# Performance work log

Hardware: AMD Instinct MI355X
Metric: run time of the kernel (lower is better)

Reference implementation:

```python
import jax, jax.numpy as jnp
import numpy as np
from jax import lax

# Module config (matches init_kwargs): mode='swta', patchwise=True, w_nrm=True, k=1, alpha=1
COUT, CIN, KH, KW = 32, 16, 3, 3
STRIDE = 1
K_TEMP = 1.0


def setup_inputs() -> dict:
    key = jax.random.key(0)
    k1, k2 = jax.random.split(key)
    x = jax.random.normal(k1, (16, CIN, 256, 256), dtype=jnp.float32)
    # xavier_normal_: std = sqrt(2/(fan_in+fan_out)), fan_in=CIN*KH*KW, fan_out=COUT*KH*KW
    std = float(np.sqrt(2.0 / (CIN * KH * KW + COUT * KH * KW)))
    weight = jax.random.normal(k2, (COUT, CIN, KH, KW), dtype=jnp.float32) * std
    bias = jnp.zeros((COUT,), dtype=jnp.float32)
    return {"x": x, "weight": weight, "bias": bias}


def _unfold(x, kh, kw, sh, sw):
    # torch F.unfold: output [B, C*kh*kw, L], patch features ordered (c, kh, kw)
    B, C, H, W = x.shape
    Ho = (H - kh) // sh + 1
    Wo = (W - kw) // sw + 1
    cols = [x[:, :, i:i + (Ho - 1) * sh + 1:sh, j:j + (Wo - 1) * sw + 1:sw]
            for i in range(kh) for j in range(kw)]  # each [B,C,Ho,Wo]
    p = jnp.stack(cols, axis=2)  # [B, C, kh*kw, Ho, Wo]
    return p.reshape(B, C * kh * kw, Ho * Wo)


def reference(x, weight, bias):
    # --- compute_activation: weight-normalized conv2d (act = Identity) ---
    nrm = jnp.sqrt((weight ** 2).sum(axis=(1, 2, 3), keepdims=True))
    nrm = jnp.where(nrm == 0, jnp.ones_like(nrm), nrm)
    w = weight / nrm
    y = lax.conv_general_dilated(
        x, w, window_strides=(STRIDE, STRIDE), padding='VALID',
        dimension_numbers=('NCHW', 'OIHW', 'NCHW')) + bias[None, :, None, None]

    # --- SWTA Hebbian update (torch: under no_grad, stored into delta_w buffer) ---
    x_unf = _unfold(x, KH, KW, STRIDE, STRIDE)               # [B, CKK, L]
    x_flat = x_unf.transpose(0, 2, 1).reshape(-1, x_unf.shape[1])  # [B*L, CKK]
    r = jax.nn.softmax(y * K_TEMP, axis=1).transpose(1, 0, 2, 3)   # [O, B, Ho, Wo]
    r_sum = jnp.abs(r).sum(axis=(1, 2, 3), keepdims=True)
    r_sum = jnp.where(r_sum == 0, jnp.ones_like(r_sum), r_sum)
    cr = (jnp.abs(r) / r_sum) * r                             # [O, B, Ho, Wo]
    cr_flat = cr.reshape(COUT, -1)                            # [O, B*L]
    dec = cr_flat.sum(axis=1, keepdims=True) * weight.reshape(COUT, -1)
    delta_w = (cr_flat @ x_flat - dec).reshape(weight.shape)  # [O, CIN, KH, KW]

    return y, delta_w
```

## Files before the change

### kernel.cpp

```cpp
#include <hip/hip_runtime.h>


typedef unsigned short ushort_t;
typedef __attribute__((ext_vector_type(8)))  short  short8v;
typedef __attribute__((ext_vector_type(4)))  float  float4v;
typedef __attribute__((ext_vector_type(16))) float  float16v;

struct __attribute__((packed, aligned(4))) f4a { float x,y,z,w; };
struct __attribute__((packed, aligned(4))) f2a { float x,y; };
struct __attribute__((packed, aligned(2))) u2a { ushort_t x,y; };

#define BATCH 16
#define CIN   16
#define H     256
#define W     256
#define HW    (H*W)
#define OCH   32
#define HO    254
#define WO    254
#define LPOS  (HO*WO)
#define YELEMS (BATCH*OCH*LPOS)
#define KFEAT 144
#define NROWS (BATCH*HO)
#define NCHUNK (NROWS*8)
#define GRIDA 1016
#define NSLAB GRIDA
#define NGRP  8
#define SLABS_PER_GRP 127

#define WS_RSUM 0
#define WS_R2   32
#define WS_ACC  64
#define WS_MODE 4672
#define WS_WNB  4680
#define WS_PART 8192
#define WS_PART2 (8192 + NSLAB*4608)
#define WS_NEED ((size_t)(WS_PART2 + NGRP*4608)*4)

__device__ __forceinline__ float bf2f(ushort_t u){
  union{unsigned u; float f;} c; c.u = ((unsigned)u) << 16; return c.f;
}
__device__ __forceinline__ ushort_t f2bf(float f){
  union{float f; unsigned u;} c; c.f = f;
  unsigned x = c.u;
  return (ushort_t)((x + 0x7fffu + ((x >> 16) & 1u)) >> 16);
}
__device__ __forceinline__ unsigned as_u(float f){
  union{float f; unsigned u;} c; c.f = f; return c.u;
}

__global__ __launch_bounds__(256) void hebb_prep(const ushort_t* __restrict__ x,
                                                 const ushort_t* __restrict__ w,
                                                 int* __restrict__ mode,
                                                 float* __restrict__ ws){
  int tid = threadIdx.x;
  int bad = 0;
  for (int i = tid; i < 16384; i += 256){
    unsigned e = ((unsigned)x[i] >> 7) & 0xFFu;
    bad |= (e >= 0x8Cu) ? 1 : 0;
  }
  unsigned long long m = __ballot(bad);
  __shared__ unsigned long long sm[4];
  __shared__ int mode_s;
  int wv = tid >> 6;
  if ((tid & 63) == 0) sm[wv] = m;
  __syncthreads();
  if (tid == 0){
    int md = ((sm[0] | sm[1] | sm[2] | sm[3]) != 0ULL) ? 1 : 0;
    *mode = md; mode_s = md;
  }
  __syncthreads();
  const int fp32 = mode_s;
  const float* wf = (const float*)w;
  __shared__ float inv_s[OCH];
  if (tid < OCH){
    float s = 0.f;
    for (int k = 0; k < KFEAT; k++){
      float v = fp32 ? wf[tid*KFEAT + k] : bf2f(w[tid*KFEAT + k]);
      s += v*v;
    }
    float nrm = sqrtf(s);
    inv_s[tid] = (nrm == 0.f) ? 1.f : (1.f/nrm);
  }
  __syncthreads();
  ushort_t* wnb = (ushort_t*)(ws + WS_WNB);
  for (int i = tid; i < 4608; i += 256){
    int o = i & 31, rest = i >> 5;
    int ij = rest >> 4, c = rest & 15;
    int k = c*9 + ij;
    float v = fp32 ? wf[o*KFEAT + k] : bf2f(w[o*KFEAT + k]);
    wnb[i] = f2bf(v * inv_s[o]);
    ws[WS_ACC + i] = 0.f;
  }
  if (tid < 64) ws[WS_RSUM + tid] = 0.f;
}

template<int FP32>
__global__ __launch_bounds__(256, 2) void hebb_passAB(
    const void* __restrict__ xv_, const void* __restrict__ bias_,
    const int* __restrict__ mode, const float* __restrict__ ws,
    float* __restrict__ rsum_g, float* __restrict__ r2sum_g,
    void* __restrict__ yout_, float* __restrict__ partial, int do_hebb){
  if (*mode != FP32) return;
  __shared__ float red_s[64];
  __shared__ float redp[4608];
  __shared__ __align__(16) ushort_t r2t[4][32*40];
  int tid = threadIdx.x;
  if (tid < 64) red_s[tid] = 0.f;
  __syncthreads();
  int wave = tid >> 6, lane = tid & 63;
  int pos = lane & 31, half = lane >> 5;
  int quad = lane >> 4, l16 = lane & 15;

  const ushort_t* wnb = (const ushort_t*)(ws + WS_WNB);
  short8v wa[9];
  #pragma unroll
  for (int ij = 0; ij < 9; ij++){
    union{ushort_t s[8]; short8v v;} pk;
    #pragma unroll
    for (int i = 0; i < 8; i++)
      pk.s[i] = wnb[(ij*16 + half*8 + i)*32 + pos];
    wa[ij] = pk.v;
  }
  float bv[16];
  #pragma unroll
  for (int r = 0; r < 16; r++){
    int och = (r&3) + 8*(r>>2) + 4*half;
    bv[r] = FP32 ? ((const float*)bias_)[och] : bf2f(((const ushort_t*)bias_)[och]);
  }
  float rsA[16];
  #pragma unroll
  for (int r = 0; r < 16; r++) rsA[r] = 0.f;
  float r2B0 = 0.f, r2B1 = 0.f;

  float4v hacc[18];
  #pragma unroll
  for (int i = 0; i < 18; i++) hacc[i] = (float4v){0.f,0.f,0.f,0.f};

  ushort_t* t2 = r2t[wave];

  for (int cc0 = blockIdx.x*4 + wave; cc0 < NCHUNK; cc0 += GRIDA*4){
    int cc = __builtin_amdgcn_readfirstlane(cc0);
    int row = cc >> 3, sub = cc & 7;
    int b = row / HO, ho = row - b*HO;
    int wo0 = sub << 5;
    int wo = wo0 + pos;
    int tail = (sub == 7);

    float16v av;
    #pragma unroll
    for (int r = 0; r < 16; r++) av[r] = bv[r];

    if (FP32 && !tail){
      const float* xp = (const float*)xv_ + (size_t)b*(CIN*HW)
                        + (size_t)(half*8)*HW + (size_t)ho*W + wo;
      #pragma unroll
      for (int ii = 0; ii < 3; ii++){
        f4a g[8];
        #pragma unroll
        for (int i2 = 0; i2 < 8; i2++)
          g[i2] = *(const f4a*)(xp + (size_t)ii*W + (size_t)i2*HW);
        #pragma unroll
        for (int jj = 0; jj < 3; jj++){
          union{unsigned u[4]; short8v v;} pk;
          #pragma unroll
          for (int k2 = 0; k2 < 4; k2++){
            float flo = (jj==0) ? g[2*k2].x   : (jj==1) ? g[2*k2].y   : g[2*k2].z;
            float fhi = (jj==0) ? g[2*k2+1].x : (jj==1) ? g[2*k2+1].y : g[2*k2+1].z;
            pk.u[k2] = __builtin_amdgcn_perm(as_u(fhi)+0x8000u, as_u(flo)+0x8000u,
                                             0x07060302u);
          }
          av = __builtin_amdgcn_mfma_f32_32x32x16_bf16(wa[ii*3+jj], pk.v, av, 0,0,0);
        }
      }
    } else {
      #pragma unroll
      for (int ij = 0; ij < 9; ij++){
        const int ii = ij/3, jj = ij - 3*ii;
        int wcol = wo + jj; wcol = (wcol < 256) ? wcol : 255;
        size_t a0 = (size_t)b*(CIN*HW) + (size_t)(half*8)*HW + (size_t)(ho+ii)*W + wcol;
        short8v bx;
        if (FP32){
          const float* xp = (const float*)xv_;
          unsigned g[8];
          #pragma unroll
          for (int i2 = 0; i2 < 8; i2++)
            g[i2] = as_u(xp[a0 + (size_t)i2*HW]) + 0x8000u;
          union{unsigned u[4]; short8v v;} pk;
          pk.u[0] = __builtin_amdgcn_perm(g[1], g[0], 0x07060302u);
          pk.u[1] = __builtin_amdgcn_perm(g[3], g[2], 0x07060302u);
          pk.u[2] = __builtin_amdgcn_perm(g[5], g[4], 0x07060302u);
          pk.u[3] = __builtin_amdgcn_perm(g[7], g[6], 0x07060302u);
          bx = pk.v;
        } else {
          const ushort_t* xp = (const ushort_t*)xv_;
          union{ushort_t s[8]; short8v v;} pk;
          #pragma unroll
          for (int i2 = 0; i2 < 8; i2++)
            pk.s[i2] = xp[a0 + (size_t)i2*HW];
          bx = pk.v;
        }
        av = __builtin_amdgcn_mfma_f32_32x32x16_bf16(wa[ij], bx, av, 0, 0, 0);
      }
    }

    int valid = (wo < WO) ? 1 : 0;
    if (valid){
      size_t yb = (size_t)b*(OCH*(size_t)LPOS) + (size_t)(half*4)*LPOS
                + (size_t)ho*WO + wo;
      #pragma unroll
      for (int r = 0; r < 16; r++){
        size_t yi = yb + (size_t)(((r&3) + 8*(r>>2)))*LPOS;
        if (FP32) ((float*)yout_)[yi] = av[r];
        else      ((ushort_t*)yout_)[yi] = f2bf(av[r]);
      }
    }

    float m = -3.0e38f;
    #pragma unroll
    for (int r = 0; r < 16; r++) m = fmaxf(m, av[r]);
    m = fmaxf(m, __shfl_xor(m, 32));
    float s = 0.f;
    #pragma unroll
    for (int r = 0; r < 16; r++){ float e = __expf(av[r] - m); av[r] = e; s += e; }
    s += __shfl_xor(s, 32);
    float inv = valid ? (1.f/s) : 0.f;

    #pragma unroll
    for (int r = 0; r < 16; r++){
      float rr = av[r]*inv;
      rsA[r] += rr;
      int och = (r&3) + 8*(r>>2) + 4*half;
      t2[och*40 + pos] = f2bf(rr*rr);
    }

    short8v a0 = *(const short8v*)(t2 + l16*40      + quad*8);
    short8v a1 = *(const short8v*)(t2 + (16+l16)*40 + quad*8);
    {
      float p0 = 0.f, p1 = 0.f;
      #pragma unroll
      for (int i = 0; i < 8; i++){
        p0 += bf2f((ushort_t)a0[i]);
        p1 += bf2f((ushort_t)a1[i]);
      }
      r2B0 += p0; r2B1 += p1;
    }

    if (do_hebb){
      int xbase = b*(CIN*HW) + ho*W + wo0;
      #pragma unroll
      for (int n = 0; n < 9; n++){
        int kh = n*16 + l16, c = kh/9, ij = kh - 9*c, ii = ij/3, jj = ij - 3*ii;
        int ko = (c*H + ii)*W + jj;
        short8v bx2;
        if (FP32){
          const float* xp = (const float*)xv_ + (size_t)(xbase + ko + quad*8);
          unsigned f[8];
          if (tail && quad == 3){
            f4a t0 = *(const f4a*)xp;
            f2a t1 = *(const f2a*)(xp + 4);
            f[0]=as_u(t0.x); f[1]=as_u(t0.y); f[2]=as_u(t0.z); f[3]=as_u(t0.w);
            f[4]=as_u(t1.x); f[5]=as_u(t1.y); f[6]=0u; f[7]=0u;
          } else {
            f4a t0 = *(const f4a*)xp;
            f4a t1 = *(const f4a*)(xp + 4);
            f[0]=as_u(t0.x); f[1]=as_u(t0.y); f[2]=as_u(t0.z); f[3]=as_u(t0.w);
            f[4]=as_u(t1.x); f[5]=as_u(t1.y); f[6]=as_u(t1.z); f[7]=as_u(t1.w);
          }
          union{unsigned u[4]; short8v v;} pk;
          pk.u[0] = __builtin_amdgcn_perm(f[1], f[0], 0x07060302u);
          pk.u[1] = __builtin_amdgcn_perm(f[3], f[2], 0x07060302u);
          pk.u[2] = __builtin_amdgcn_perm(f[5], f[4], 0x07060302u);
          pk.u[3] = __builtin_amdgcn_perm(f[7], f[6], 0x07060302u);
          bx2 = pk.v;
        } else {
          const ushort_t* xp = (const ushort_t*)xv_ + (size_t)(xbase + ko + quad*8);
          union{ushort_t s[8]; short8v v;} pk;
          if (tail && quad == 3){
            u2a u0 = *(const u2a*)xp, u1 = *(const u2a*)(xp+2), u2 = *(const u2a*)(xp+4);
            pk.s[0]=u0.x; pk.s[1]=u0.y; pk.s[2]=u1.x; pk.s[3]=u1.y;
            pk.s[4]=u2.x; pk.s[5]=u2.y; pk.s[6]=0; pk.s[7]=0;
          } else {
            u2a u0 = *(const u2a*)xp,   u1 = *(const u2a*)(xp+2);
            u2a u2 = *(const u2a*)(xp+4), u3 = *(const u2a*)(xp+6);
            pk.s[0]=u0.x; pk.s[1]=u0.y; pk.s[2]=u1.x; pk.s[3]=u1.y;
            pk.s[4]=u2.x; pk.s[5]=u2.y; pk.s[6]=u3.x; pk.s[7]=u3.y;
          }
          bx2 = pk.v;
        }
        hacc[n]   = __builtin_amdgcn_mfma_f32_16x16x32_bf16(a0, bx2, hacc[n],   0,0,0);
        hacc[9+n] = __builtin_amdgcn_mfma_f32_16x16x32_bf16(a1, bx2, hacc[9+n], 0,0,0);
      }
    }
  }

  #pragma unroll
  for (int r = 0; r < 16; r++){
    float a = rsA[r];
    #pragma unroll
    for (int off = 1; off < 32; off <<= 1)
      a += __shfl_xor(a, off);
    if (pos == 0){
      int och = (r&3) + 8*(r>>2) + 4*half;
      atomicAdd(&red_s[och], a);
    }
  }
  r2B0 += __shfl_xor(r2B0, 16); r2B0 += __shfl_xor(r2B0, 32);
  r2B1 += __shfl_xor(r2B1, 16); r2B1 += __shfl_xor(r2B1, 32);
  if (lane < 16){
    atomicAdd(&red_s[32 + lane],      r2B0);
    atomicAdd(&red_s[32 + 16 + lane], r2B1);
  }
  __syncthreads();
  if (tid < 32)      atomicAdd(rsum_g  + tid,      red_s[tid]);
  else if (tid < 64) atomicAdd(r2sum_g + (tid-32), red_s[tid]);

  if (do_hebb){
    for (int wv = 0; wv < 4; wv++){
      if (wave == wv){
        #pragma unroll
        for (int mi = 0; mi < 2; mi++)
          #pragma unroll
          for (int n = 0; n < 9; n++)
            #pragma unroll
            for (int rg = 0; rg < 4; rg++){
              int o  = mi*16 + quad*4 + rg;
              int kh = n*16 + l16;
              if (wv == 0) redp[o*KFEAT + kh]  = hacc[mi*9+n][rg];
              else         redp[o*KFEAT + kh] += hacc[mi*9+n][rg];
            }
      }
      __syncthreads();
    }
    float* myp = partial + (size_t)blockIdx.x*4608;
    for (int i = tid; i < 4608; i += 256) myp[i] = redp[i];
  }
}

__global__ __launch_bounds__(256) void hebb_red(const float* __restrict__ partial,
                                                float* __restrict__ partial2){
  int t = blockIdx.x*256 + threadIdx.x;
  if (t >= NGRP*4608) return;
  int g = t / 4608, col = t - g*4608;
  const float* p = partial + (size_t)g*SLABS_PER_GRP*4608 + col;
  float s0=0.f, s1=0.f, s2=0.f, s3=0.f;
  int j = 0;
  for (; j + 4 <= SLABS_PER_GRP; j += 4){
    s0 += p[(size_t)(j  )*4608];
    s1 += p[(size_t)(j+1)*4608];
    s2 += p[(size_t)(j+2)*4608];
    s3 += p[(size_t)(j+3)*4608];
  }
  for (; j < SLABS_PER_GRP; j++) s0 += p[(size_t)j*4608];
  partial2[t] = ((s0+s1)+(s2+s3));
}

template<int FP32>
__global__ __launch_bounds__(256) void hebb_passB_fb(
    const void* __restrict__ xv_, const int* __restrict__ mode,
    const float* __restrict__ ws, const void* __restrict__ ybf_,
    float* __restrict__ acc_g){
  if (*mode != FP32) return;
  __shared__ __align__(16) ushort_t crs[32*128];
  __shared__ __align__(16) ushort_t xs[144*128];
  __shared__ float rsinv_s[32];
  int tid = threadIdx.x;
  if (tid < 32){
    float rs = ws[WS_RSUM + tid];
    rsinv_s[tid] = (rs == 0.f) ? 1.f : (1.f/rs);
  }
  __syncthreads();

  float4v av[18];
  #pragma unroll
  for (int i = 0; i < 18; i++) av[i] = (float4v){0.f,0.f,0.f,0.f};
  int wave = tid >> 6, lane = tid & 63;
  int quad = lane >> 4, l16 = lane & 15;
  int t = tid & 127, kh0 = tid >> 7;

  for (int s = blockIdx.x; s < NROWS*2; s += (int)gridDim.x){
    int row = s >> 1, half = s & 1;
    int b = row / HO, ho = row - b*HO;
    int wo0 = half << 7;
    int tlen = half ? (WO - 128) : 128;
    size_t xoff = (size_t)b*(CIN*HW) + (size_t)ho*W + wo0;
    bool tvalid = t < tlen;

    #pragma unroll
    for (int it = 0; it < 72; it++){
      const int kh = 2*it + kh0;
      const int c = kh/9, ij = kh - 9*c, ii = ij/3, jj = ij - 3*ii;
      size_t gi = xoff + (size_t)(c*H + ii)*W + jj + t;
      ushort_t val;
      if (FP32) val = tvalid ? f2bf(((const float*)xv_)[gi]) : (ushort_t)0;
      else      val = tvalid ? ((const ushort_t*)xv_)[gi]    : (ushort_t)0;
      xs[kh*128 + t] = val;
    }
    if (tid < 128){
      if (tvalid){
        float r[32];
        size_t yb = (size_t)b*(OCH*(size_t)LPOS) + (size_t)ho*WO + wo0 + tid;
        float m = -3.0e38f;
        #pragma unroll
        for (int o = 0; o < 32; o++){
          float v = FP32 ? ((const float*)ybf_)[yb + (size_t)o*LPOS]
                         : bf2f(((const ushort_t*)ybf_)[yb + (size_t)o*LPOS]);
          r[o] = v; m = fmaxf(m, v);
        }
        float ssum = 0.f;
        #pragma unroll
        for (int o = 0; o < 32; o++){ r[o] = __expf(r[o]-m); ssum += r[o]; }
        float inv = 1.f/ssum;
        #pragma unroll
        for (int o = 0; o < 32; o++) r[o] *= inv;
        #pragma unroll
        for (int o = 0; o < 32; o++) crs[o*128 + tid] = f2bf(r[o]*r[o]*rsinv_s[o]);
      } else {
        #pragma unroll
        for (int o = 0; o < 32; o++) crs[o*128 + tid] = 0;
      }
    }
    __syncthreads();

    int t0 = wave*32;
    short8v a0 = *(const short8v*)(crs + l16*128      + t0 + quad*8);
    short8v a1 = *(const short8v*)(crs + (16+l16)*128 + t0 + quad*8);
    #pragma unroll
    for (int n = 0; n < 9; n++){
      short8v bfr = *(const short8v*)(xs + (n*16 + l16)*128 + t0 + quad*8);
      av[n]   = __builtin_amdgcn_mfma_f32_16x16x32_bf16(a0, bfr, av[n],   0,0,0);
      av[9+n] = __builtin_amdgcn_mfma_f32_16x16x32_bf16(a1, bfr, av[9+n], 0,0,0);
    }
    __syncthreads();
  }

  #pragma unroll
  for (int mi = 0; mi < 2; mi++)
    #pragma unroll
    for (int n = 0; n < 9; n++)
      #pragma unroll
      for (int rg = 0; rg < 4; rg++){
        int o  = mi*16 + quad*4 + rg;
        int kh = n*16 + l16;
        atomicAdd(acc_g + o*KFEAT + kh, av[mi*9+n][rg]);
      }
}

__global__ __launch_bounds__(256) void hebb_fin(const ushort_t* __restrict__ w,
    const int* __restrict__ mode, const float* __restrict__ ws,
    const float* __restrict__ partial2, int use_rbuf, void* __restrict__ dout){
  int tid = blockIdx.x*256 + threadIdx.x;
  if (tid >= 4608) return;
  const int fp32 = *mode;
  int o = tid / KFEAT;
  float rs = ws[WS_RSUM + o];
  rs = (rs == 0.f) ? 1.f : rs;
  float base;
  if (use_rbuf){
    float s = 0.f;
    #pragma unroll
    for (int j = 0; j < NGRP; j++)
      s += partial2[(size_t)j*4608 + tid];
    base = s / rs;
  } else {
    base = ws[WS_ACC + tid];
  }
  float crsum = ws[WS_R2 + o] / rs;
  float wv = fp32 ? ((const float*)w)[tid] : bf2f(w[tid]);
  float d = base - crsum * wv;
  if (fp32) ((float*)dout)[(size_t)YELEMS + tid] = d;
  else      ((ushort_t*)dout)[(size_t)YELEMS + tid] = f2bf(d);
}

extern "C" void kernel_launch(void* const* d_in, const int* in_sizes, int n_in,
                              void* d_out, int out_size, void* d_ws, size_t ws_size,
                              hipStream_t stream){
  const void* x    = d_in[0];
  const ushort_t* w = (const ushort_t*)d_in[1];
  const void* bias = d_in[2];
  float* ws   = (float*)d_ws;
  int*   mode = (int*)(ws + WS_MODE);
  float* part = ws + WS_PART;
  float* part2 = ws + WS_PART2;
  int use_rbuf = (ws_size >= WS_NEED) ? 1 : 0;

  hebb_prep<<<1, 256, 0, stream>>>((const ushort_t*)x, w, mode, ws);
  hebb_passAB<0><<<GRIDA, 256, 0, stream>>>(x, bias, mode, ws,
                                            ws + WS_RSUM, ws + WS_R2, d_out,
                                            part, use_rbuf);
  hebb_passAB<1><<<GRIDA, 256, 0, stream>>>(x, bias, mode, ws,
                                            ws + WS_RSUM, ws + WS_R2, d_out,
                                            part, use_rbuf);
  if (use_rbuf){
    hebb_red<<<144, 256, 0, stream>>>(part, part2);
  } else {
    hebb_passB_fb<0><<<512, 256, 0, stream>>>(x, mode, ws, d_out, ws + WS_ACC);
    hebb_passB_fb<1><<<512, 256, 0, stream>>>(x, mode, ws, d_out, ws + WS_ACC);
  }
  hebb_fin<<<18, 256, 0, stream>>>(w, mode, ws, part2, use_rbuf, d_out);
}
```

Measured before the change: 339.6 us.

## Stage per-wave input tile in LDS via global_load_lds for conv and Hebbian passes

Each wave now copies the 16-channel x 3-row x 36-column fp32 input window for its chunk into LDS with direct global-to-LDS loads. Both the convolution MFMA operands and the Hebbian outer-product operands are then built from that shared tile instead of being fetched from global memory twice. The Hebbian reduction buffer is aliased onto the tile storage, which lowers total LDS use. The cost is a full vmcnt wait before compute, plus possible LDS bank conflicts from the strided tile reads, and the aliasing is only safe if the tile is no longer needed when the reduction runs.

```diff
diff --git a/kernel.cpp b/kernel.cpp
--- a/kernel.cpp
+++ b/kernel.cpp
@@ -28,6 +28,8 @@
 #define NGRP  8
 #define SLABS_PER_GRP 127
 
+#define TCOLS 36
+
 #define WS_RSUM 0
 #define WS_R2   32
 #define WS_ACC  64
@@ -47,6 +49,11 @@
 }
 __device__ __forceinline__ unsigned as_u(float f){
   union{float f; unsigned u;} c; c.f = f; return c.u;
+}
+__device__ __forceinline__ void gload_lds16(const float* g, void* l){
+  __builtin_amdgcn_global_load_lds(
+      (const __attribute__((address_space(1))) void*)g,
+      (__attribute__((address_space(3))) void*)l, 16, 0, 0);
 }
 
 __global__ __launch_bounds__(256) void hebb_prep(const ushort_t* __restrict__ x,
@@ -102,9 +109,10 @@
     float* __restrict__ rsum_g, float* __restrict__ r2sum_g,
     void* __restrict__ yout_, float* __restrict__ partial, int do_hebb){
   if (*mode != FP32) return;
+  __shared__ __align__(16) float xtile[4][1792];
+  __shared__ __align__(16) ushort_t r2t[4][32*40];
   __shared__ float red_s[64];
-  __shared__ float redp[4608];
-  __shared__ __align__(16) ushort_t r2t[4][32*40];
+  float* redp = &xtile[0][0];
   int tid = threadIdx.x;
   if (tid < 64) red_s[tid] = 0.f;
   __syncthreads();
@@ -133,11 +141,22 @@
   for (int r = 0; r < 16; r++) rsA[r] = 0.f;
   float r2B0 = 0.f, r2B1 = 0.f;
 
+  int goff[7], qcol[7];
+  #pragma unroll
+  for (int i = 0; i < 7; i++){
+    int slot = i*64 + lane; slot = (slot > 431) ? 431 : slot;
+    int rr = slot/9, q = slot - 9*rr;
+    int c = rr/3, ii = rr - 3*c;
+    goff[i] = c*HW + ii*W;
+    qcol[i] = q*4;
+  }
+
   float4v hacc[18];
   #pragma unroll
   for (int i = 0; i < 18; i++) hacc[i] = (float4v){0.f,0.f,0.f,0.f};
 
   ushort_t* t2 = r2t[wave];
+  float* tw = &xtile[wave][0];
 
   for (int cc0 = blockIdx.x*4 + wave; cc0 < NCHUNK; cc0 += GRIDA*4){
     int cc = __builtin_amdgcn_readfirstlane(cc0);
@@ -151,27 +170,28 @@
     #pragma unroll
     for (int r = 0; r < 16; r++) av[r] = bv[r];
 
-    if (FP32 && !tail){
-      const float* xp = (const float*)xv_ + (size_t)b*(CIN*HW)
-                        + (size_t)(half*8)*HW + (size_t)ho*W + wo;
-      #pragma unroll
-      for (int ii = 0; ii < 3; ii++){
-        f4a g[8];
+    if (FP32){
+      const float* xb = (const float*)xv_ + (size_t)b*(CIN*HW) + (size_t)ho*W;
+      #pragma unroll
+      for (int i = 0; i < 7; i++){
+        int col = wo0 + qcol[i]; col = (col > 252) ? 252 : col;
+        gload_lds16(xb + goff[i] + col, (char*)tw + i*1024);
+      }
+      asm volatile("s_waitcnt vmcnt(0)" ::: "memory");
+
+      #pragma unroll
+      for (int ij = 0; ij < 9; ij++){
+        const int ii = ij/3, jj = ij - 3*ii;
+        unsigned g[8];
         #pragma unroll
         for (int i2 = 0; i2 < 8; i2++)
-          g[i2] = *(const f4a*)(xp + (size_t)ii*W + (size_t)i2*HW);
-        #pragma unroll
-        for (int jj = 0; jj < 3; jj++){
-          union{unsigned u[4]; short8v v;} pk;
-          #pragma unroll
-          for (int k2 = 0; k2 < 4; k2++){
-            float flo = (jj==0) ? g[2*k2].x   : (jj==1) ? g[2*k2].y   : g[2*k2].z;
-            float fhi = (jj==0) ? g[2*k2+1].x : (jj==1) ? g[2*k2+1].y : g[2*k2+1].z;
-            pk.u[k2] = __builtin_amdgcn_perm(as_u(fhi)+0x8000u, as_u(flo)+0x8000u,
-                                             0x07060302u);
-          }
-          av = __builtin_amdgcn_mfma_f32_32x32x16_bf16(wa[ii*3+jj], pk.v, av, 0,0,0);
-        }
+          g[i2] = as_u(tw[((half*8 + i2)*3 + ii)*TCOLS + pos + jj]) + 0x8000u;
+        union{unsigned u[4]; short8v v;} pk;
+        pk.u[0] = __builtin_amdgcn_perm(g[1], g[0], 0x07060302u);
+        pk.u[1] = __builtin_amdgcn_perm(g[3], g[2], 0x07060302u);
+        pk.u[2] = __builtin_amdgcn_perm(g[5], g[4], 0x07060302u);
+        pk.u[3] = __builtin_amdgcn_perm(g[7], g[6], 0x07060302u);
+        av = __builtin_amdgcn_mfma_f32_32x32x16_bf16(wa[ij], pk.v, av, 0, 0, 0);
       }
     } else {
       #pragma unroll
@@ -179,28 +199,12 @@
         const int ii = ij/3, jj = ij - 3*ii;
         int wcol = wo + jj; wcol = (wcol < 256) ? wcol : 255;
         size_t a0 = (size_t)b*(CIN*HW) + (size_t)(half*8)*HW + (size_t)(ho+ii)*W + wcol;
-        short8v bx;
-        if (FP32){
-          const float* xp = (const float*)xv_;
-          unsigned g[8];
-          #pragma unroll
-          for (int i2 = 0; i2 < 8; i2++)
-            g[i2] = as_u(xp[a0 + (size_t)i2*HW]) + 0x8000u;
-          union{unsigned u[4]; short8v v;} pk;
-          pk.u[0] = __builtin_amdgcn_perm(g[1], g[0], 0x07060302u);
-          pk.u[1] = __builtin_amdgcn_perm(g[3], g[2], 0x07060302u);
-          pk.u[2] = __builtin_amdgcn_perm(g[5], g[4], 0x07060302u);
-          pk.u[3] = __builtin_amdgcn_perm(g[7], g[6], 0x07060302u);
-          bx = pk.v;
-        } else {
-          const ushort_t* xp = (const ushort_t*)xv_;
-          union{ushort_t s[8]; short8v v;} pk;
-          #pragma unroll
-          for (int i2 = 0; i2 < 8; i2++)
-            pk.s[i2] = xp[a0 + (size_t)i2*HW];
-          bx = pk.v;
-        }
-        av = __builtin_amdgcn_mfma_f32_32x32x16_bf16(wa[ij], bx, av, 0, 0, 0);
+        const ushort_t* xp = (const ushort_t*)xv_;
+        union{ushort_t s[8]; short8v v;} pk;
+        #pragma unroll
+        for (int i2 = 0; i2 < 8; i2++)
+          pk.s[i2] = xp[a0 + (size_t)i2*HW];
+        av = __builtin_amdgcn_mfma_f32_32x32x16_bf16(wa[ij], pk.v, av, 0, 0, 0);
       }
     }
 
@@ -247,33 +251,28 @@
     }
 
     if (do_hebb){
-      int xbase = b*(CIN*HW) + ho*W + wo0;
-      #pragma unroll
-      for (int n = 0; n < 9; n++){
-        int kh = n*16 + l16, c = kh/9, ij = kh - 9*c, ii = ij/3, jj = ij - 3*ii;
-        int ko = (c*H + ii)*W + jj;
-        short8v bx2;
-        if (FP32){
-          const float* xp = (const float*)xv_ + (size_t)(xbase + ko + quad*8);
+      if (FP32){
+        #pragma unroll
+        for (int n = 0; n < 9; n++){
+          int kh = n*16 + l16, c = kh/9, ij2 = kh - 9*c, ii = ij2/3, jj = ij2 - 3*ii;
+          const float* hp = tw + (c*3 + ii)*TCOLS + jj + quad*8;
           unsigned f[8];
-          if (tail && quad == 3){
-            f4a t0 = *(const f4a*)xp;
-            f2a t1 = *(const f2a*)(xp + 4);
-            f[0]=as_u(t0.x); f[1]=as_u(t0.y); f[2]=as_u(t0.z); f[3]=as_u(t0.w);
-            f[4]=as_u(t1.x); f[5]=as_u(t1.y); f[6]=0u; f[7]=0u;
-          } else {
-            f4a t0 = *(const f4a*)xp;
-            f4a t1 = *(const f4a*)(xp + 4);
-            f[0]=as_u(t0.x); f[1]=as_u(t0.y); f[2]=as_u(t0.z); f[3]=as_u(t0.w);
-            f[4]=as_u(t1.x); f[5]=as_u(t1.y); f[6]=as_u(t1.z); f[7]=as_u(t1.w);
-          }
+          #pragma unroll
+          for (int i = 0; i < 8; i++) f[i] = as_u(hp[i]);
           union{unsigned u[4]; short8v v;} pk;
           pk.u[0] = __builtin_amdgcn_perm(f[1], f[0], 0x07060302u);
           pk.u[1] = __builtin_amdgcn_perm(f[3], f[2], 0x07060302u);
           pk.u[2] = __builtin_amdgcn_perm(f[5], f[4], 0x07060302u);
           pk.u[3] = __builtin_amdgcn_perm(f[7], f[6], 0x07060302u);
-          bx2 = pk.v;
-        } else {
+          hacc[n]   = __builtin_amdgcn_mfma_f32_16x16x32_bf16(a0, pk.v, hacc[n],   0,0,0);
+          hacc[9+n] = __builtin_amdgcn_mfma_f32_16x16x32_bf16(a1, pk.v, hacc[9+n], 0,0,0);
+        }
+      } else {
+        int xbase = b*(CIN*HW) + ho*W + wo0;
+        #pragma unroll
+        for (int n = 0; n < 9; n++){
+          int kh = n*16 + l16, c = kh/9, ij2 = kh - 9*c, ii = ij2/3, jj = ij2 - 3*ii;
+          int ko = (c*H + ii)*W + jj;
           const ushort_t* xp = (const ushort_t*)xv_ + (size_t)(xbase + ko + quad*8);
           union{ushort_t s[8]; short8v v;} pk;
           if (tail && quad == 3){
@@ -286,10 +285,9 @@
             pk.s[0]=u0.x; pk.s[1]=u0.y; pk.s[2]=u1.x; pk.s[3]=u1.y;
             pk.s[4]=u2.x; pk.s[5]=u2.y; pk.s[6]=u3.x; pk.s[7]=u3.y;
           }
-          bx2 = pk.v;
+          hacc[n]   = __builtin_amdgcn_mfma_f32_16x16x32_bf16(a0, pk.v, hacc[n],   0,0,0);
+          hacc[9+n] = __builtin_amdgcn_mfma_f32_16x16x32_bf16(a1, pk.v, hacc[9+n], 0,0,0);
         }
-        hacc[n]   = __builtin_amdgcn_mfma_f32_16x16x32_bf16(a0, bx2, hacc[n],   0,0,0);
-        hacc[9+n] = __builtin_amdgcn_mfma_f32_16x16x32_bf16(a1, bx2, hacc[9+n], 0,0,0);
       }
     }
   }
```

Measured after the change: 287.2 us. 15.5% less time.
